# Kernel optimization log

Measured on AMD Instinct MI355X. Metric: run time of the kernel, lower is better.

The kernel has to match this reference:

```python
import jax, jax.numpy as jnp
import numpy as np
from jax.scipy.linalg import solve_triangular

JITTER = 1e-4  # matches init jitter


def kernel_ard(x1, x2, log_ls, log_sf):
    # ARD RBF kernel: sf * exp(-0.5 * || (x1 - x2) / ls ||^2)
    # x1: (b,H,N,D), x2: (b,H,M,D); log_ls: (H,D); log_sf: (H,1)
    inv_ls = jnp.exp(-log_ls)[None, :, None, :]
    a = x1 * inv_ls
    b = x2 * inv_ls
    d2 = (jnp.sum(a * a, -1)[..., :, None]
          - 2.0 * jnp.einsum('bhnd,bhmd->bhnm', a, b)
          + jnp.sum(b * b, -1)[..., None, :])
    sf = jnp.exp(log_sf)[None, :, :, None]  # (1,H,1,1)
    return sf * jnp.exp(-0.5 * d2)


def sgp_forward(x, cur_k, eps, W_qkv, log_sf, log_ls, v_ind, s_sqrt_ltri, log_s_sqrt_diag, W_O_w, W_O_b):
    B, L, hdim = x.shape
    H, vd = log_ls.shape
    M = cur_k.shape[1]
    S = eps.shape[2]

    # fc_qkv + head split (q and v_gamma interleaved per head)
    qkv = (x @ W_qkv.T).reshape(B, L, H, 2 * vd).transpose(0, 2, 1, 3)  # (B,H,L,2vd)
    q, v_gamma = qkv[..., :vd], qkv[..., vd:]

    # inducing keys: first hdim rows of fc_qkv weight applied to cur_k
    W_qk = W_qkv[:hdim].reshape(H, vd, hdim)
    k_beta = jnp.einsum('hdk,mk->hmd', W_qk, cur_k[0])[None]  # (1,H,M,vd)
    k_beta_b = jnp.broadcast_to(k_beta, (B, H, M, vd))
    v_beta = jnp.transpose(v_ind, (1, 0, 2, 3))               # (1,H,M,vd)
    log_ssqrt = jnp.transpose(log_s_sqrt_diag, (1, 0, 2, 3))  # (1,H,vd,M)

    K_qq = kernel_ard(q, q, log_ls, log_sf)               # (B,H,L,L)
    K_qk_beta = kernel_ard(q, k_beta_b, log_ls, log_sf)   # (B,H,L,M)
    K_kk = kernel_ard(k_beta, k_beta, log_ls, log_sf)     # (1,H,M,M)
    K_kq = jnp.swapaxes(K_qk_beta, -1, -2)                # (B,H,M,L)

    eyeM = jnp.eye(M, dtype=x.dtype)
    s_sqrt = jnp.exp(log_ssqrt)
    # diag_embed(s_sqrt) + strictly-lower-tri part of s_sqrt_ltri
    s_local = eyeM * s_sqrt[..., :, None] + jnp.tril(jnp.transpose(s_sqrt_ltri, (1, 0, 2, 3, 4)), -1)  # (1,H,vd,M,M)

    chol = jnp.linalg.cholesky(K_kk + JITTER * eyeM)      # (1,H,M,M)
    cholB = jnp.broadcast_to(chol, (B, H, M, M))
    v1 = solve_triangular(cholB, K_kq, lower=True)        # (B,H,M,L)
    v2 = solve_triangular(cholB, K_kq @ v_gamma, lower=True)  # (B,H,M,vd)
    v3 = jnp.einsum('bhml,hdmn->bhdln', v1, s_local[0])   # (B,H,vd,L,M)

    mean1 = K_qq @ v_gamma                                # (B,H,L,vd)
    mean = mean1 - jnp.einsum('bhml,bhmd->bhld', v1, v2) + K_qk_beta @ v_beta

    covar1 = jnp.diagonal(K_qq, axis1=-2, axis2=-1)[:, :, None, :, None]  # (B,H,1,L,1)
    v3sq = jnp.swapaxes(jnp.sum(v3 * v3, -1), 2, 3)[:, :, None]           # (B,H,1,L,vd)
    v1sq = jnp.sum(v1 * v1, 2)[:, :, None, :, None]                       # (B,H,1,L,1)
    chol_covar = jnp.sqrt(covar1 + v3sq - v1sq)           # (B,H,1,L,vd)

    samples = mean[:, :, None] + chol_covar * eps         # (B,H,S,L,vd)
    samples = samples.transpose(0, 2, 3, 1, 4).reshape(B, S, L, H * vd)
    out = samples @ W_O_w.T + W_O_b                       # (B,S,L,hdim); dropout p=0 -> identity

    # KL divergence (training path)
    kl = jnp.asarray(-0.5 * M * vd * H, dtype=x.dtype)
    kl = kl + 0.5 * jnp.sum(s_local * s_local)
    kl = kl + 0.5 * jnp.einsum('ohmd,ohmn,ohnd->', v_beta, K_kk, v_beta)
    per_b = jnp.sum(v_gamma * mean1, axis=(1, 2, 3)) - jnp.sum(v2 * v2, axis=(1, 2, 3))
    kl = kl + 0.5 * jnp.mean(per_b)
    kl = kl - jnp.sum(log_ssqrt)
    return out, kl


def setup_inputs():
    key = jax.random.key(0)
    ks = jax.random.split(key, 10)
    B, L, H, vd, M, S = 8, 512, 8, 64, 64, 2
    hdim = H * vd
    return {
        "x": jax.random.normal(ks[0], (B, L, hdim), jnp.float32),
        "cur_k": jax.random.normal(ks[1], (1, M, hdim), jnp.float32),
        "eps": jax.random.normal(ks[2], (B, H, S, L, vd), jnp.float32),
        "W_qkv": jax.random.normal(ks[3], (2 * hdim, hdim), jnp.float32) / np.float32(np.sqrt(hdim)),
        "log_sf": jnp.zeros((H, 1), jnp.float32),
        "log_ls": jax.random.normal(ks[4], (H, vd), jnp.float32),
        "v_ind": jax.random.normal(ks[5], (H, 1, M, vd), jnp.float32),
        "s_sqrt_ltri": 0.1 * jax.random.normal(ks[6], (H, 1, vd, M, M), jnp.float32),
        "log_s_sqrt_diag": jax.random.normal(ks[7], (H, 1, vd, M), jnp.float32),
        "W_O_w": jax.random.normal(ks[8], (hdim, hdim), jnp.float32) / np.float32(np.sqrt(hdim)),
        "W_O_b": jax.random.normal(ks[9], (hdim,), jnp.float32),
    }


def reference(x, cur_k, eps, W_qkv, log_sf, log_ls, v_ind, s_sqrt_ltri, log_s_sqrt_diag, W_O_w, W_O_b):
    return sgp_forward(x, cur_k, eps, W_qkv, log_sf, log_ls, v_ind, s_sqrt_ltri, log_s_sqrt_diag, W_O_w, W_O_b)
```

## Files before the change

kernel.cpp:

```cpp
#include <hip/hip_runtime.h>
#include <math.h>


using bf16x8 = __attribute__((ext_vector_type(8))) short;
using f32x4  = __attribute__((ext_vector_type(4))) float;

static const size_t OFF_QS   = 0;
static const size_t OFF_VG   = OFF_QS   + 2097152;
static const size_t OFF_QN   = OFF_VG   + 2097152;
static const size_t OFF_KBS  = OFF_QN   + 32768;
static const size_t OFF_KBN  = OFF_KBS  + 32768;
static const size_t OFF_LINV = OFF_KBN  + 512;
static const size_t OFF_V1   = OFF_LINV + 32768;
static const size_t OFF_V1SQ = OFF_V1   + 2097152;
static const size_t OFF_MEAN = OFF_V1SQ + 32768;
static const size_t OFF_V2   = OFF_MEAN + 2097152;
static const size_t OFF_V1H  = OFF_V2   + 262144;
static const size_t OFF_V1L  = OFF_V1H  + 1048576;
static const size_t OFF_STH  = OFF_V1L  + 1048576;
static const size_t OFF_STL  = OFF_STH  + 1048576;
static const size_t OFF_V3   = OFF_STL  + 1048576;
static const size_t OFF_WOH  = OFF_V3   + 2097152;
static const size_t OFF_WOL  = OFF_WOH  + 131072;
static const size_t OFF_KLD  = OFF_WOL  + 131072;

__device__ __forceinline__ unsigned short f2bf(float x) {
  unsigned u = __float_as_uint(x);
  u += 0x7FFFu + ((u >> 16) & 1u);
  return (unsigned short)(u >> 16);
}
__device__ __forceinline__ float bf2f(unsigned short s) {
  return __uint_as_float(((unsigned)s) << 16);
}
__device__ __forceinline__ void splitbf(float x, unsigned short& h, unsigned short& l) {
  h = f2bf(x);
  l = f2bf(x - bf2f(h));
}

__device__ __forceinline__ void load_tile_t(float* dst, const float* src, int ld) {
  int t = threadIdx.x;
  int r = t >> 2;
  int c0 = (t & 3) * 16;
#pragma unroll
  for (int q = 0; q < 4; ++q) {
    float4 v = *(const float4*)(src + (size_t)r * ld + c0 + q * 4);
    int c = c0 + q * 4;
    dst[(c + 0) * 68 + r] = v.x;
    dst[(c + 1) * 68 + r] = v.y;
    dst[(c + 2) * 68 + r] = v.z;
    dst[(c + 3) * 68 + r] = v.w;
  }
}
__device__ __forceinline__ void load_tile_n(float* dst, const float* src, int ld) {
  int t = threadIdx.x;
  int r = t >> 2;
  int c0 = (t & 3) * 16;
#pragma unroll
  for (int q = 0; q < 4; ++q) {
    float4 v = *(const float4*)(src + (size_t)r * ld + c0 + q * 4);
    *(float4*)(dst + r * 68 + c0 + q * 4) = v;
  }
}
__device__ __forceinline__ void mma64(const float* aT, const float* bT, int tr, int tn,
                                      float acc[4][4]) {
#pragma unroll 16
  for (int k = 0; k < 64; ++k) {
    float4 av = *(const float4*)(aT + k * 68 + tr);
    float4 bv = *(const float4*)(bT + k * 68 + tn);
    float a[4] = {av.x, av.y, av.z, av.w};
    float b[4] = {bv.x, bv.y, bv.z, bv.w};
#pragma unroll
    for (int i = 0; i < 4; ++i)
#pragma unroll
      for (int j = 0; j < 4; ++j) acc[i][j] = fmaf(a[i], b[j], acc[i][j]);
  }
}
__device__ __forceinline__ void mma64_dual(const float* aT, const float* b1T,
                                           const float* b2T, int tr, int tn,
                                           float acc1[4][4], float acc2[4][4]) {
#pragma unroll 8
  for (int k = 0; k < 64; ++k) {
    float4 av = *(const float4*)(aT + k * 68 + tr);
    float4 b1 = *(const float4*)(b1T + k * 68 + tn);
    float4 b2 = *(const float4*)(b2T + k * 68 + tn);
    float a[4] = {av.x, av.y, av.z, av.w};
    float p[4] = {b1.x, b1.y, b1.z, b1.w};
    float q[4] = {b2.x, b2.y, b2.z, b2.w};
#pragma unroll
    for (int i = 0; i < 4; ++i)
#pragma unroll
      for (int j = 0; j < 4; ++j) {
        acc1[i][j] = fmaf(a[i], p[j], acc1[i][j]);
        acc2[i][j] = fmaf(a[i], q[j], acc2[i][j]);
      }
  }
}

__global__ __launch_bounds__(256) void gemm0(
    const float* __restrict__ A, const float* __restrict__ Bm,
    float* __restrict__ qs, float* __restrict__ vg, const float* __restrict__ lls,
    float* __restrict__ qn) {
  __shared__ float As[16][68];
  __shared__ float Bs[16][68];
  const int t = threadIdx.x;
  const int r0 = blockIdx.x * 64;
  const int n0 = blockIdx.y * 64;
  const int lr = t >> 2;
  const int lk = (t & 3) * 4;
  const int tr = (t >> 4) * 4;
  const int tn = (t & 15) * 4;
  const float* Ap = A + (size_t)(r0 + lr) * 512 + lk;
  const float* Bp = Bm + (size_t)(n0 + lr) * 512 + lk;
  float acc[4][4] = {};
  for (int k0 = 0; k0 < 512; k0 += 16) {
    float4 a4 = *(const float4*)(Ap + k0);
    float4 b4 = *(const float4*)(Bp + k0);
    As[lk + 0][lr] = a4.x; As[lk + 1][lr] = a4.y; As[lk + 2][lr] = a4.z; As[lk + 3][lr] = a4.w;
    Bs[lk + 0][lr] = b4.x; Bs[lk + 1][lr] = b4.y; Bs[lk + 2][lr] = b4.z; Bs[lk + 3][lr] = b4.w;
    __syncthreads();
#pragma unroll
    for (int k = 0; k < 16; ++k) {
      float4 av = *(const float4*)&As[k][tr];
      float4 bv = *(const float4*)&Bs[k][tn];
      float a[4] = {av.x, av.y, av.z, av.w};
      float b[4] = {bv.x, bv.y, bv.z, bv.w};
#pragma unroll
      for (int i = 0; i < 4; ++i)
#pragma unroll
        for (int j = 0; j < 4; ++j) acc[i][j] = fmaf(a[i], b[j], acc[i][j]);
    }
    __syncthreads();
  }
  const int h = n0 >> 7;
  const bool isq = (n0 & 64) == 0;
  if (isq) {
    float invls[4];
#pragma unroll
    for (int j = 0; j < 4; ++j) invls[j] = __expf(-lls[h * 64 + tn + j]);
    float* red = &As[0][0];
#pragma unroll
    for (int i = 0; i < 4; ++i) {
      int r = r0 + tr + i;
      int b = r >> 9, l = r & 511;
      float4 o;
      o.x = acc[i][0] * invls[0];
      o.y = acc[i][1] * invls[1];
      o.z = acc[i][2] * invls[2];
      o.w = acc[i][3] * invls[3];
      *(float4*)(qs + (((size_t)(b * 8 + h)) * 512 + l) * 64 + tn) = o;
      red[(tr + i) * 17 + (t & 15)] = o.x * o.x + o.y * o.y + o.z * o.z + o.w * o.w;
    }
    __syncthreads();
    if (t < 64) {
      float s = 0.f;
#pragma unroll
      for (int g = 0; g < 16; ++g) s += red[t * 17 + g];
      int r = r0 + t;
      int b = r >> 9, l = r & 511;
      qn[(b * 8 + h) * 512 + l] = s;
    }
  } else {
#pragma unroll
    for (int i = 0; i < 4; ++i) {
      int r = r0 + tr + i;
      int b = r >> 9, l = r & 511;
      float4 o = {acc[i][0], acc[i][1], acc[i][2], acc[i][3]};
      *(float4*)(vg + (((size_t)(b * 8 + h)) * 512 + l) * 64 + tn) = o;
    }
  }
}

__global__ __launch_bounds__(256) void k2_kbeta(const float* __restrict__ W,
                                                const float* __restrict__ ckg,
                                                const float* __restrict__ log_ls,
                                                float* __restrict__ kbs,
                                                float* __restrict__ kbn) {
  __shared__ float ck[512];
  __shared__ float kb[64];
  int h = blockIdx.x >> 6, m = blockIdx.x & 63;
  int t = threadIdx.x;
  ck[t] = ckg[m * 512 + t];
  ck[t + 256] = ckg[m * 512 + t + 256];
  __syncthreads();
  int w = t >> 6, lane = t & 63;
  for (int d = w; d < 64; d += 4) {
    const float* row = W + (size_t)(h * 64 + d) * 512;
    float p = 0.f;
    for (int k = lane; k < 512; k += 64) p = fmaf(row[k], ck[k], p);
#pragma unroll
    for (int off = 32; off > 0; off >>= 1) p += __shfl_down(p, off);
    if (lane == 0) {
      float v = p * __expf(-log_ls[h * 64 + d]);
      kbs[(size_t)h * 4096 + m * 64 + d] = v;
      kb[d] = v;
    }
  }
  __syncthreads();
  if (w == 0) {
    float v = kb[lane];
    v *= v;
#pragma unroll
    for (int off = 32; off > 0; off >>= 1) v += __shfl_down(v, off);
    if (lane == 0) kbn[h * 64 + m] = v;
  }
}

__global__ __launch_bounds__(64) void k3_chol(const float* __restrict__ kbs,
                                              const float* __restrict__ kbn,
                                              const float* __restrict__ vind,
                                              const float* __restrict__ log_sf,
                                              float* __restrict__ linv_g,
                                              double* __restrict__ klbuf) {
  __shared__ float Am[64][65];
  __shared__ float Bm[64][65];
  __shared__ float kn[64];
  int h = blockIdx.x;
  int t = threadIdx.x;
  for (int m = 0; m < 64; ++m) Bm[m][t] = kbs[(size_t)h * 4096 + m * 64 + t];
  kn[t] = kbn[h * 64 + t];
  float lsf = log_sf[h];
  __syncthreads();
  float nh = -0.5f * kn[t] + lsf;
  for (int n = 0; n < 64; ++n) {
    float dt = 0.f;
#pragma unroll 8
    for (int d = 0; d < 64; ++d) dt = fmaf(Bm[t][d], Bm[n][d], dt);
    Am[t][n] = __expf(dt + nh - 0.5f * kn[n]);
  }
  __syncthreads();
  for (int m = 0; m < 64; ++m) Bm[m][t] = vind[(size_t)h * 4096 + m * 64 + t];
  __syncthreads();
  float s = 0.f;
  for (int m = 0; m < 64; ++m) {
    float tt = 0.f;
    for (int n = 0; n < 64; ++n) tt = fmaf(Am[m][n], Bm[n][t], tt);
    s = fmaf(Bm[m][t], tt, s);
  }
#pragma unroll
  for (int off = 32; off > 0; off >>= 1) s += __shfl_down(s, off);
  if (t == 0) atomicAdd(&klbuf[1], 0.5 * (double)s);
  __syncthreads();
  Am[t][t] += 1e-4f;
  __syncthreads();
  for (int k = 0; k < 64; ++k) {
    if (t == k) Am[k][k] = sqrtf(Am[k][k]);
    __syncthreads();
    if (t > k) Am[t][k] /= Am[k][k];
    __syncthreads();
    if (t > k) {
      float f = Am[t][k];
      for (int j = k + 1; j <= t; ++j) Am[t][j] = fmaf(-f, Am[j][k], Am[t][j]);
    }
    __syncthreads();
  }
  for (int i = 0; i < t; ++i) Bm[i][t] = 0.f;
  Bm[t][t] = 1.f / Am[t][t];
  for (int i = t + 1; i < 64; ++i) {
    float a = 0.f;
    for (int j = t; j < i; ++j) a = fmaf(Am[i][j], Bm[j][t], a);
    Bm[i][t] = -a / Am[i][i];
  }
  __syncthreads();
  for (int m = 0; m < 64; ++m) linv_g[(size_t)h * 4096 + m * 64 + t] = Bm[m][t];
}

__global__ __launch_bounds__(256) void ks_build(const float* __restrict__ ltri,
                                                const float* __restrict__ ldiag,
                                                unsigned short* __restrict__ sth,
                                                unsigned short* __restrict__ stl,
                                                double* __restrict__ klbuf) {
  __shared__ float r1[256], r2[256];
  int hd = blockIdx.x;
  int t = threadIdx.x;
  float p2 = 0.f, pl = 0.f;
  for (int i = t; i < 4096; i += 256) {
    int n = i >> 6, m = i & 63;
    float v;
    if (m == n) v = __expf(ldiag[hd * 64 + m]);
    else if (m > n) v = ltri[(size_t)hd * 4096 + m * 64 + n];
    else v = 0.f;
    unsigned short h, l;
    splitbf(v, h, l);
    sth[(size_t)hd * 4096 + i] = h;
    stl[(size_t)hd * 4096 + i] = l;
    p2 = fmaf(0.5f * v, v, p2);
  }
  if (t < 64) pl = ldiag[hd * 64 + t];
  r1[t] = p2;
  r2[t] = pl;
  __syncthreads();
  for (int sft = 128; sft > 0; sft >>= 1) {
    if (t < sft) { r1[t] += r1[t + sft]; r2[t] += r2[t + sft]; }
    __syncthreads();
  }
  if (t == 0) {
    atomicAdd(&klbuf[0], (double)r1[0]);
    atomicAdd(&klbuf[2], (double)r2[0]);
  }
}

__global__ __launch_bounds__(256) void kconv_wo(const float* __restrict__ w,
                                                unsigned short* __restrict__ wh,
                                                unsigned short* __restrict__ wl) {
  int i = blockIdx.x * 256 + threadIdx.x;
  float v = w[i];
  unsigned short h, l;
  splitbf(v, h, l);
  wh[i] = h;
  wl[i] = l;
}

__global__ __launch_bounds__(256) void k4_fused(
    const float* __restrict__ qs, const float* __restrict__ qn,
    const float* __restrict__ kbs, const float* __restrict__ kbn,
    const float* __restrict__ linv, const float* __restrict__ vind,
    const float* __restrict__ log_sf, float* __restrict__ v1,
    unsigned short* __restrict__ v1h, unsigned short* __restrict__ v1l,
    float* __restrict__ v1sq, float* __restrict__ meanbuf) {
  extern __shared__ float lds[];
  float* qsT = lds;
  float* kbT = lds + 4352;
  float* liT = lds + 2 * 4352;
  float* vbN = lds + 3 * 4352;
  float* red = lds + 4 * 4352;
  __shared__ float qn_s[64], kbn_s[64];
  const int lt = blockIdx.x, bh = blockIdx.y;
  const int h = bh & 7;
  const int t = threadIdx.x;
  const int l0 = lt * 64;
  const int tr = (t >> 4) * 4, tn = (t & 15) * 4;
  load_tile_t(qsT, qs + ((size_t)bh * 512 + l0) * 64, 64);
  load_tile_t(kbT, kbs + (size_t)h * 4096, 64);
  load_tile_t(liT, linv + (size_t)h * 4096, 64);
  load_tile_n(vbN, vind + (size_t)h * 4096, 64);
  if (t < 64) {
    qn_s[t] = qn[bh * 512 + l0 + t];
    kbn_s[t] = kbn[h * 64 + t];
  }
  __syncthreads();
  float acc[4][4] = {};
  mma64(qsT, kbT, tr, tn, acc);
  const float lsf = log_sf[h];
  float arow[4], acol[4];
#pragma unroll
  for (int i = 0; i < 4; ++i) arow[i] = -0.5f * qn_s[tr + i];
#pragma unroll
  for (int j = 0; j < 4; ++j) acol[j] = -0.5f * kbn_s[tn + j] + lsf;
  float kv[4][4];
#pragma unroll
  for (int i = 0; i < 4; ++i)
#pragma unroll
    for (int j = 0; j < 4; ++j) kv[i][j] = __expf(acc[i][j] + arow[i] + acol[j]);
  __syncthreads();
#pragma unroll
  for (int i = 0; i < 4; ++i)
#pragma unroll
    for (int j = 0; j < 4; ++j) qsT[(tn + j) * 68 + (tr + i)] = kv[i][j];
  __syncthreads();
  float a2[4][4] = {};
  float a3[4][4] = {};
  mma64_dual(qsT, liT, vbN, tr, tn, a2, a3);
#pragma unroll
  for (int i = 0; i < 4; ++i) {
    const size_t rowbase = ((size_t)bh * 512 + l0 + tr + i) * 64 + tn;
    float4 o = {a2[i][0], a2[i][1], a2[i][2], a2[i][3]};
    *(float4*)(v1 + rowbase) = o;
    short4 sh, sl;
    unsigned short hh, ll;
    splitbf(o.x, hh, ll); sh.x = (short)hh; sl.x = (short)ll;
    splitbf(o.y, hh, ll); sh.y = (short)hh; sl.y = (short)ll;
    splitbf(o.z, hh, ll); sh.z = (short)hh; sl.z = (short)ll;
    splitbf(o.w, hh, ll); sh.w = (short)hh; sl.w = (short)ll;
    *(short4*)(v1h + rowbase) = sh;
    *(short4*)(v1l + rowbase) = sl;
    red[(tr + i) * 17 + (t & 15)] =
        a2[i][0] * a2[i][0] + a2[i][1] * a2[i][1] + a2[i][2] * a2[i][2] + a2[i][3] * a2[i][3];
    float4 o3 = {a3[i][0], a3[i][1], a3[i][2], a3[i][3]};
    *(float4*)(meanbuf + rowbase) = o3;
  }
  __syncthreads();
  if (t < 64) {
    float s2 = 0.f;
#pragma unroll
    for (int g = 0; g < 16; ++g) s2 += red[t * 17 + g];
    v1sq[bh * 512 + l0 + t] = s2;
  }
}

__global__ __launch_bounds__(256) void k5_v2(const float* __restrict__ v1,
                                             const float* __restrict__ vg,
                                             float* __restrict__ v2,
                                             double* __restrict__ klbuf) {
  __shared__ float v1t[64 * 68];
  __shared__ float vgt[64 * 68];
  __shared__ float redp[256];
  const int bh = blockIdx.x;
  const int b = bh >> 3;
  const int t = threadIdx.x;
  const int tr = (t >> 4) * 4, tn = (t & 15) * 4;
  float acc[4][4] = {};
  for (int c0 = 0; c0 < 512; c0 += 64) {
    __syncthreads();
    load_tile_n(v1t, v1 + ((size_t)bh * 512 + c0) * 64, 64);
    load_tile_n(vgt, vg + ((size_t)bh * 512 + c0) * 64, 64);
    __syncthreads();
    mma64(v1t, vgt, tr, tn, acc);
  }
  float p = 0.f;
#pragma unroll
  for (int i = 0; i < 4; ++i) {
    float4 o = {acc[i][0], acc[i][1], acc[i][2], acc[i][3]};
    *(float4*)(v2 + ((size_t)bh * 64 + tr + i) * 64 + tn) = o;
    p += acc[i][0] * acc[i][0] + acc[i][1] * acc[i][1] + acc[i][2] * acc[i][2] +
         acc[i][3] * acc[i][3];
  }
  redp[t] = p;
  __syncthreads();
  if (t < 64) {
    float s = redp[t] + redp[t + 64] + redp[t + 128] + redp[t + 192];
#pragma unroll
    for (int off = 32; off > 0; off >>= 1) s += __shfl_down(s, off);
    if (t == 0) atomicAdd(&klbuf[11 + b], (double)s);
  }
}

__global__ __launch_bounds__(256) void k6_mean1(const float* __restrict__ qs,
                                                const float* __restrict__ qn,
                                                const float* __restrict__ vg,
                                                const float* __restrict__ log_sf,
                                                float* __restrict__ meanbuf,
                                                double* __restrict__ klbuf) {
  extern __shared__ float lds[];
  float* qrT = lds;
  float* qcT = lds + 4352;
  float* sT = lds + 2 * 4352;
  float* vgN = lds + 3 * 4352;
  __shared__ float qn_r[64], qn_c[64], redp[256];
  const int lt = blockIdx.x, bh = blockIdx.y;
  const int b = bh >> 3, h = bh & 7;
  const int l0 = lt * 64;
  const int t = threadIdx.x;
  const int tr = (t >> 4) * 4, tn = (t & 15) * 4;
  load_tile_t(qrT, qs + ((size_t)bh * 512 + l0) * 64, 64);
  if (t < 64) qn_r[t] = qn[bh * 512 + l0 + t];
  const float lsf = log_sf[h];
  float acc[4][4] = {};
  for (int c0 = 0; c0 < 512; c0 += 64) {
    __syncthreads();
    load_tile_t(qcT, qs + ((size_t)bh * 512 + c0) * 64, 64);
    load_tile_n(vgN, vg + ((size_t)bh * 512 + c0) * 64, 64);
    if (t < 64) qn_c[t] = qn[bh * 512 + c0 + t];
    __syncthreads();
    float dt[4][4] = {};
    mma64(qrT, qcT, tr, tn, dt);
    float arow[4], acol[4];
#pragma unroll
    for (int i = 0; i < 4; ++i) arow[i] = -0.5f * qn_r[tr + i];
#pragma unroll
    for (int j = 0; j < 4; ++j) acol[j] = -0.5f * qn_c[tn + j] + lsf;
#pragma unroll
    for (int i = 0; i < 4; ++i)
#pragma unroll
      for (int j = 0; j < 4; ++j)
        sT[(tn + j) * 68 + (tr + i)] = __expf(dt[i][j] + arow[i] + acol[j]);
    __syncthreads();
    mma64(sT, vgN, tr, tn, acc);
  }
  float pb = 0.f;
#pragma unroll
  for (int i = 0; i < 4; ++i) {
    size_t rowbase = ((size_t)bh * 512 + l0 + tr + i) * 64 + tn;
    float4 vgr = *(const float4*)(vg + rowbase);
    float4 mb = *(const float4*)(meanbuf + rowbase);
    pb += acc[i][0] * vgr.x + acc[i][1] * vgr.y + acc[i][2] * vgr.z + acc[i][3] * vgr.w;
    mb.x += acc[i][0]; mb.y += acc[i][1]; mb.z += acc[i][2]; mb.w += acc[i][3];
    *(float4*)(meanbuf + rowbase) = mb;
  }
  redp[t] = pb;
  __syncthreads();
  if (t < 64) {
    float s = redp[t] + redp[t + 64] + redp[t + 128] + redp[t + 192];
#pragma unroll
    for (int off = 32; off > 0; off >>= 1) s += __shfl_down(s, off);
    if (t == 0) atomicAdd(&klbuf[3 + b], (double)s);
  }
}

__global__ __launch_bounds__(256) void k10_mfma(const unsigned short* __restrict__ v1h,
                                                const unsigned short* __restrict__ sth,
                                                float* __restrict__ v3) {
  const int bh = blockIdx.x;
  const int l0 = blockIdx.y * 128;
  const int dz = blockIdx.z;
  const int h = bh & 7;
  const int t = threadIdx.x;
  const int wv = t >> 6;
  const int lane = t & 63;
  const int lr = lane & 15;
  const int kq = lane >> 4;
  const int lbase = l0 + wv * 32;
  bf16x8 a[2][2];
#pragma unroll
  for (int s = 0; s < 2; ++s)
#pragma unroll
    for (int kk = 0; kk < 2; ++kk)
      a[s][kk] = *(const bf16x8*)(v1h + ((size_t)bh * 512 + lbase + s * 16 + lr) * 64 +
                                  kk * 32 + kq * 8);
  const unsigned short* sbase = sth + (size_t)(h * 64 + dz * 16) * 4096;
  bf16x8 b[2][6];
#pragma unroll
  for (int ns = 0; ns < 4; ++ns)
    b[0][ns] = *(const bf16x8*)(sbase + (size_t)(ns * 16 + lr) * 64 + 32 + kq * 8);
#pragma unroll
  for (int ns = 0; ns < 2; ++ns)
    b[0][4 + ns] = *(const bf16x8*)(sbase + (size_t)(ns * 16 + lr) * 64 + kq * 8);
#pragma unroll
  for (int dd = 0; dd < 16; ++dd) {
    const int cur = dd & 1, nxt = cur ^ 1;
    if (dd < 15) {
      const unsigned short* sb = sbase + (size_t)(dd + 1) * 4096;
#pragma unroll
      for (int ns = 0; ns < 4; ++ns)
        b[nxt][ns] = *(const bf16x8*)(sb + (size_t)(ns * 16 + lr) * 64 + 32 + kq * 8);
#pragma unroll
      for (int ns = 0; ns < 2; ++ns)
        b[nxt][4 + ns] = *(const bf16x8*)(sb + (size_t)(ns * 16 + lr) * 64 + kq * 8);
    }
#pragma unroll
    for (int s = 0; s < 2; ++s) {
      f32x4 acc[4];
#pragma unroll
      for (int ns = 0; ns < 4; ++ns) acc[ns] = (f32x4){0.f, 0.f, 0.f, 0.f};
#pragma unroll
      for (int ns = 0; ns < 4; ++ns)
        acc[ns] = __builtin_amdgcn_mfma_f32_16x16x32_bf16(a[s][1], b[cur][ns], acc[ns], 0, 0, 0);
#pragma unroll
      for (int ns = 0; ns < 2; ++ns)
        acc[ns] = __builtin_amdgcn_mfma_f32_16x16x32_bf16(a[s][0], b[cur][4 + ns], acc[ns], 0, 0, 0);
      float sum[4];
#pragma unroll
      for (int r = 0; r < 4; ++r)
        sum[r] = acc[0][r] * acc[0][r] + acc[1][r] * acc[1][r] + acc[2][r] * acc[2][r] +
                 acc[3][r] * acc[3][r];
#pragma unroll
      for (int off = 1; off <= 8; off <<= 1)
#pragma unroll
        for (int r = 0; r < 4; ++r) sum[r] += __shfl_xor(sum[r], off);
      if (lr == 0) {
        const int d = dz * 16 + dd;
        const size_t base = ((size_t)(bh * 64 + d)) * 512 + lbase + s * 16 + kq * 4;
        v3[base + 0] = sum[0];
        v3[base + 1] = sum[1];
        v3[base + 2] = sum[2];
        v3[base + 3] = sum[3];
      }
    }
  }
}

__global__ __launch_bounds__(256) void k8_samples(
    const float* __restrict__ v1, const float* __restrict__ v2,
    const float* __restrict__ meanbuf, const float* __restrict__ v3,
    const float* __restrict__ v1sq, const float* __restrict__ eps,
    const float* __restrict__ log_sf, unsigned short* __restrict__ smph,
    unsigned short* __restrict__ smpl) {
  extern __shared__ float lds[];
  float* v1T = lds;
  float* v2N = lds + 4352;
  float* v3T = lds + 2 * 4352;
  __shared__ float v1sq_s[64];
  const int lt = blockIdx.x, bh = blockIdx.y;
  const int b = bh >> 3, h = bh & 7;
  const int l0 = lt * 64;
  const int t = threadIdx.x;
  const int tr = (t >> 4) * 4, tn = (t & 15) * 4;
  load_tile_t(v1T, v1 + ((size_t)bh * 512 + l0) * 64, 64);
  load_tile_n(v2N, v2 + (size_t)bh * 4096, 64);
  load_tile_n(v3T, v3 + (size_t)bh * 64 * 512 + l0, 512);
  if (t < 64) v1sq_s[t] = v1sq[bh * 512 + l0 + t];
  __syncthreads();
  float acc[4][4] = {};
  mma64(v1T, v2N, tr, tn, acc);
  const float sf = __expf(log_sf[h]);
#pragma unroll
  for (int i = 0; i < 4; ++i) {
    const int l = l0 + tr + i;
    size_t mbase = ((size_t)bh * 512 + l) * 64 + tn;
    float4 mb = *(const float4*)(meanbuf + mbase);
    float mean[4] = {mb.x - acc[i][0], mb.y - acc[i][1], mb.z - acc[i][2], mb.w - acc[i][3]};
    float cc[4];
#pragma unroll
    for (int j = 0; j < 4; ++j) {
      float var = sf + v3T[(tn + j) * 68 + (tr + i)] - v1sq_s[tr + i];
      cc[j] = sqrtf(fmaxf(var, 0.f));
    }
#pragma unroll
    for (int s2 = 0; s2 < 2; ++s2) {
      float4 ep = *(const float4*)(eps + (((size_t)bh * 2 + s2) * 512 + l) * 64 + tn);
      float o[4];
      o[0] = mean[0] + cc[0] * ep.x;
      o[1] = mean[1] + cc[1] * ep.y;
      o[2] = mean[2] + cc[2] * ep.z;
      o[3] = mean[3] + cc[3] * ep.w;
      short4 sh, sl;
      unsigned short hh, ll;
      splitbf(o[0], hh, ll); sh.x = (short)hh; sl.x = (short)ll;
      splitbf(o[1], hh, ll); sh.y = (short)hh; sl.y = (short)ll;
      splitbf(o[2], hh, ll); sh.z = (short)hh; sl.z = (short)ll;
      splitbf(o[3], hh, ll); sh.w = (short)hh; sl.w = (short)ll;
      const size_t obase = (((size_t)(b * 2 + s2) * 512 + l) * 512) + h * 64 + tn;
      *(short4*)(smph + obase) = sh;
      *(short4*)(smpl + obase) = sl;
    }
  }
}

__global__ __launch_bounds__(256) void gemm1_mfma(const unsigned short* __restrict__ smph,
                                                  const unsigned short* __restrict__ smpl,
                                                  const unsigned short* __restrict__ woh,
                                                  const unsigned short* __restrict__ wol,
                                                  const float* __restrict__ bias,
                                                  float* __restrict__ out) {
  const int r0 = blockIdx.x * 64;
  const int n0 = blockIdx.y * 64;
  const int t = threadIdx.x;
  const int wv = t >> 6;
  const int lane = t & 63;
  const int lr = lane & 15;
  const int kq = lane >> 4;
  const size_t arow = ((size_t)(r0 + wv * 16 + lr)) * 512;
  f32x4 acc[4];
#pragma unroll
  for (int ns = 0; ns < 4; ++ns) acc[ns] = (f32x4){0.f, 0.f, 0.f, 0.f};
  for (int ks = 0; ks < 16; ++ks) {
    const int kb = ks * 32 + kq * 8;
    bf16x8 ah = *(const bf16x8*)(smph + arow + kb);
    bf16x8 al = *(const bf16x8*)(smpl + arow + kb);
#pragma unroll
    for (int ns = 0; ns < 4; ++ns) {
      const size_t brow = ((size_t)(n0 + ns * 16 + lr)) * 512 + kb;
      bf16x8 bh8 = *(const bf16x8*)(woh + brow);
      bf16x8 bl8 = *(const bf16x8*)(wol + brow);
      acc[ns] = __builtin_amdgcn_mfma_f32_16x16x32_bf16(ah, bh8, acc[ns], 0, 0, 0);
      acc[ns] = __builtin_amdgcn_mfma_f32_16x16x32_bf16(ah, bl8, acc[ns], 0, 0, 0);
      acc[ns] = __builtin_amdgcn_mfma_f32_16x16x32_bf16(al, bh8, acc[ns], 0, 0, 0);
    }
  }
#pragma unroll
  for (int ns = 0; ns < 4; ++ns) {
    const int outc = n0 + ns * 16 + lr;
    const float bc = bias[outc];
    const int rbase = r0 + wv * 16 + kq * 4;
#pragma unroll
    for (int r = 0; r < 4; ++r) {
      out[(size_t)(rbase + r) * 512 + outc] = acc[ns][r] + bc;
    }
  }
}

__global__ void kfin(const double* __restrict__ klbuf, float* __restrict__ dout) {
  if (threadIdx.x == 0 && blockIdx.x == 0) {
    double pb = 0.0;
    for (int b = 0; b < 8; ++b) pb += klbuf[3 + b] - klbuf[11 + b];
    double kl = -16384.0 + klbuf[0] + klbuf[1] - klbuf[2] + pb / 16.0;
    dout[4194304] = (float)kl;
  }
}

extern "C" void kernel_launch(void* const* d_in, const int* in_sizes, int n_in,
                              void* d_out, int out_size, void* d_ws, size_t ws_size,
                              hipStream_t stream) {
  (void)in_sizes; (void)n_in; (void)out_size; (void)ws_size;
  const float* x     = (const float*)d_in[0];
  const float* cur_k = (const float*)d_in[1];
  const float* eps   = (const float*)d_in[2];
  const float* W_qkv = (const float*)d_in[3];
  const float* lsf   = (const float*)d_in[4];
  const float* lls   = (const float*)d_in[5];
  const float* vind  = (const float*)d_in[6];
  const float* ltri  = (const float*)d_in[7];
  const float* ldia  = (const float*)d_in[8];
  const float* Wo    = (const float*)d_in[9];
  const float* Wob   = (const float*)d_in[10];
  float* out = (float*)d_out;
  float* ws = (float*)d_ws;
  float* qs   = ws + OFF_QS;
  float* vg   = ws + OFF_VG;
  float* qn   = ws + OFF_QN;
  float* kbs  = ws + OFF_KBS;
  float* kbn  = ws + OFF_KBN;
  float* linv = ws + OFF_LINV;
  float* v1   = ws + OFF_V1;
  float* v1s  = ws + OFF_V1SQ;
  float* mean = ws + OFF_MEAN;
  float* v2   = ws + OFF_V2;
  float* v3   = ws + OFF_V3;
  unsigned short* v1h = (unsigned short*)(ws + OFF_V1H);
  unsigned short* v1l = (unsigned short*)(ws + OFF_V1L);
  unsigned short* sth = (unsigned short*)(ws + OFF_STH);
  unsigned short* stl = (unsigned short*)(ws + OFF_STL);
  unsigned short* woh = (unsigned short*)(ws + OFF_WOH);
  unsigned short* wol = (unsigned short*)(ws + OFF_WOL);
  unsigned short* smph = (unsigned short*)(ws + OFF_QS);
  unsigned short* smpl = (unsigned short*)(ws + OFF_VG);
  double* kld = (double*)(ws + OFF_KLD);

  hipMemsetAsync(kld, 0, 32 * sizeof(double), stream);
  gemm0<<<dim3(64, 16), 256, 0, stream>>>(x, W_qkv, qs, vg, lls, qn);
  k2_kbeta<<<512, 256, 0, stream>>>(W_qkv, cur_k, lls, kbs, kbn);
  k3_chol<<<8, 64, 0, stream>>>(kbs, kbn, vind, lsf, linv, kld);
  ks_build<<<512, 256, 0, stream>>>(ltri, ldia, sth, stl, kld);
  kconv_wo<<<1024, 256, 0, stream>>>(Wo, woh, wol);
  k4_fused<<<dim3(8, 64), 256, 73984, stream>>>(qs, qn, kbs, kbn, linv, vind, lsf,
                                                v1, v1h, v1l, v1s, mean);
  k5_v2<<<64, 256, 0, stream>>>(v1, vg, v2, kld);
  k6_mean1<<<dim3(8, 64), 256, 69632, stream>>>(qs, qn, vg, lsf, mean, kld);
  k10_mfma<<<dim3(64, 4, 4), 256, 0, stream>>>(v1h, sth, v3);
  k8_samples<<<dim3(8, 64), 256, 52224, stream>>>(v1, v2, mean, v3, v1s, eps, lsf,
                                                  smph, smpl);
  gemm1_mfma<<<dim3(128, 8), 256, 0, stream>>>(smph, smpl, woh, wol, Wob, out);
  kfin<<<1, 64, 0, stream>>>(kld, out);
}
```

Before: 611.9 us.

## Split Cholesky into parallel build and register-resident factor-invert; drop unused bf16 low parts

The single 64-thread Cholesky kernel becomes two kernels. A 256-thread kernel builds K_kk and the KL quadratic term with more parallelism. A second kernel does the Cholesky factorisation and computes the inverse at the same time, keeping each column in registers, so the serial triangular-inverse loop is gone. It also stops computing and storing the bf16 low-part buffers for v1 and S, which k10 apparently never read, cutting global writes. The extra launch and a round-trip through a kkk workspace buffer are the cost, along with heavy register use (128 floats per thread) in the factor kernel.

Measured after the change: 567.7 us. -7.2%, faster.

```diff
diff --git a/kernel.cpp b/kernel.cpp
--- a/kernel.cpp
+++ b/kernel.cpp
@@ -18,8 +18,9 @@
 static const size_t OFF_V1H  = OFF_V2   + 262144;
 static const size_t OFF_V1L  = OFF_V1H  + 1048576;
 static const size_t OFF_STH  = OFF_V1L  + 1048576;
-static const size_t OFF_STL  = OFF_STH  + 1048576;
-static const size_t OFF_V3   = OFF_STL  + 1048576;
+static const size_t OFF_KKK  = OFF_STH  + 1048576;
+static const size_t OFF_PAD0 = OFF_KKK  + 32768;
+static const size_t OFF_V3   = OFF_PAD0 + 1015808;
 static const size_t OFF_WOH  = OFF_V3   + 2097152;
 static const size_t OFF_WOL  = OFF_WOH  + 131072;
 static const size_t OFF_KLD  = OFF_WOL  + 131072;
@@ -205,69 +206,110 @@
   }
 }
 
-__global__ __launch_bounds__(64) void k3_chol(const float* __restrict__ kbs,
-                                              const float* __restrict__ kbn,
-                                              const float* __restrict__ vind,
-                                              const float* __restrict__ log_sf,
-                                              float* __restrict__ linv_g,
-                                              double* __restrict__ klbuf) {
-  __shared__ float Am[64][65];
-  __shared__ float Bm[64][65];
+__global__ __launch_bounds__(256) void k3a_build(const float* __restrict__ kbs,
+                                                 const float* __restrict__ kbn,
+                                                 const float* __restrict__ vind,
+                                                 const float* __restrict__ log_sf,
+                                                 float* __restrict__ kkk,
+                                                 double* __restrict__ klbuf) {
+  __shared__ float Bm[64 * 68];
+  __shared__ float Vb[64 * 68];
+  __shared__ float Am[64 * 68];
   __shared__ float kn[64];
-  int h = blockIdx.x;
-  int t = threadIdx.x;
-  for (int m = 0; m < 64; ++m) Bm[m][t] = kbs[(size_t)h * 4096 + m * 64 + t];
-  kn[t] = kbn[h * 64 + t];
-  float lsf = log_sf[h];
-  __syncthreads();
-  float nh = -0.5f * kn[t] + lsf;
-  for (int n = 0; n < 64; ++n) {
-    float dt = 0.f;
-#pragma unroll 8
-    for (int d = 0; d < 64; ++d) dt = fmaf(Bm[t][d], Bm[n][d], dt);
-    Am[t][n] = __expf(dt + nh - 0.5f * kn[n]);
-  }
-  __syncthreads();
-  for (int m = 0; m < 64; ++m) Bm[m][t] = vind[(size_t)h * 4096 + m * 64 + t];
-  __syncthreads();
-  float s = 0.f;
-  for (int m = 0; m < 64; ++m) {
-    float tt = 0.f;
-    for (int n = 0; n < 64; ++n) tt = fmaf(Am[m][n], Bm[n][t], tt);
-    s = fmaf(Bm[m][t], tt, s);
-  }
-#pragma unroll
-  for (int off = 32; off > 0; off >>= 1) s += __shfl_down(s, off);
-  if (t == 0) atomicAdd(&klbuf[1], 0.5 * (double)s);
-  __syncthreads();
-  Am[t][t] += 1e-4f;
-  __syncthreads();
+  __shared__ float redp[256];
+  const int h = blockIdx.x;
+  const int t = threadIdx.x;
+  load_tile_n(Bm, kbs + (size_t)h * 4096, 64);
+  load_tile_n(Vb, vind + (size_t)h * 4096, 64);
+  if (t < 64) kn[t] = kbn[h * 64 + t];
+  const float lsf = log_sf[h];
+  __syncthreads();
+  {
+    const int m = t >> 2, q = t & 3;
+    float rowm[64];
+#pragma unroll
+    for (int d = 0; d < 64; ++d) rowm[d] = Bm[m * 68 + d];
+    const float cm = -0.5f * kn[m] + lsf;
+#pragma unroll
+    for (int nn = 0; nn < 16; ++nn) {
+      const int n = q + nn * 4;
+      float dt = 0.f;
+#pragma unroll
+      for (int d = 0; d < 64; ++d) dt = fmaf(rowm[d], Bm[n * 68 + d], dt);
+      Am[m * 68 + n] = __expf(dt + cm - 0.5f * kn[n]);
+    }
+  }
+  __syncthreads();
+  {
+    const int d = t & 63, q2 = t >> 6;
+    float sp = 0.f;
+#pragma unroll
+    for (int mm = 0; mm < 16; ++mm) {
+      const int m = q2 * 16 + mm;
+      float tt = 0.f;
+#pragma unroll
+      for (int n = 0; n < 64; ++n) tt = fmaf(Am[m * 68 + n], Vb[n * 68 + d], tt);
+      sp = fmaf(Vb[m * 68 + d], tt, sp);
+    }
+    redp[t] = sp;
+  }
+  __syncthreads();
+  for (int sft = 128; sft > 0; sft >>= 1) {
+    if (t < sft) redp[t] += redp[t + sft];
+    __syncthreads();
+  }
+  if (t == 0) atomicAdd(&klbuf[1], 0.5 * (double)redp[0]);
+#pragma unroll
+  for (int rep = 0; rep < 16; ++rep) {
+    const int i = rep * 256 + t;
+    const int m = i >> 6, n = i & 63;
+    kkk[(size_t)h * 4096 + i] = Am[m * 68 + n] + (m == n ? 1e-4f : 0.f);
+  }
+}
+
+__global__ __launch_bounds__(64) void k3b_cholinv(const float* __restrict__ kkk,
+                                                  float* __restrict__ linv_g) {
+  __shared__ float colk[64];
+  __shared__ float rinv_s;
+  const int h = blockIdx.x;
+  const int t = threadIdx.x;
+  float a[64], x[64];
+#pragma unroll
+  for (int i = 0; i < 64; ++i) a[i] = kkk[(size_t)h * 4096 + i * 64 + t];
+#pragma unroll
+  for (int i = 0; i < 64; ++i) x[i] = (i == t) ? 1.f : 0.f;
+#pragma unroll
   for (int k = 0; k < 64; ++k) {
-    if (t == k) Am[k][k] = sqrtf(Am[k][k]);
-    __syncthreads();
-    if (t > k) Am[t][k] /= Am[k][k];
-    __syncthreads();
-    if (t > k) {
-      float f = Am[t][k];
-      for (int j = k + 1; j <= t; ++j) Am[t][j] = fmaf(-f, Am[j][k], Am[t][j]);
-    }
-    __syncthreads();
-  }
-  for (int i = 0; i < t; ++i) Bm[i][t] = 0.f;
-  Bm[t][t] = 1.f / Am[t][t];
-  for (int i = t + 1; i < 64; ++i) {
-    float a = 0.f;
-    for (int j = t; j < i; ++j) a = fmaf(Am[i][j], Bm[j][t], a);
-    Bm[i][t] = -a / Am[i][i];
-  }
-  __syncthreads();
-  for (int m = 0; m < 64; ++m) linv_g[(size_t)h * 4096 + m * 64 + t] = Bm[m][t];
+    if (t == k) {
+      const float dk = sqrtf(a[k]);
+      const float ri = 1.f / dk;
+      rinv_s = ri;
+#pragma unroll
+      for (int i = k + 1; i < 64; ++i) {
+        a[i] *= ri;
+        colk[i] = a[i];
+      }
+    }
+    __syncthreads();
+    const float ri = rinv_s;
+    const float fc = (t > k) ? colk[t] : 0.f;
+    const float xk = x[k] * ri;
+    x[k] = xk;
+#pragma unroll
+    for (int i = k + 1; i < 64; ++i) {
+      const float ci = colk[i];
+      a[i] = fmaf(-fc, ci, a[i]);
+      x[i] = fmaf(-ci, xk, x[i]);
+    }
+    __syncthreads();
+  }
+#pragma unroll
+  for (int m = 0; m < 64; ++m) linv_g[(size_t)h * 4096 + m * 64 + t] = x[m];
 }
 
 __global__ __launch_bounds__(256) void ks_build(const float* __restrict__ ltri,
                                                 const float* __restrict__ ldiag,
                                                 unsigned short* __restrict__ sth,
-                                                unsigned short* __restrict__ stl,
                                                 double* __restrict__ klbuf) {
   __shared__ float r1[256], r2[256];
   int hd = blockIdx.x;
@@ -279,10 +321,7 @@
     if (m == n) v = __expf(ldiag[hd * 64 + m]);
     else if (m > n) v = ltri[(size_t)hd * 4096 + m * 64 + n];
     else v = 0.f;
-    unsigned short h, l;
-    splitbf(v, h, l);
-    sth[(size_t)hd * 4096 + i] = h;
-    stl[(size_t)hd * 4096 + i] = l;
+    sth[(size_t)hd * 4096 + i] = f2bf(v);
     p2 = fmaf(0.5f * v, v, p2);
   }
   if (t < 64) pl = ldiag[hd * 64 + t];
@@ -315,7 +354,7 @@
     const float* __restrict__ kbs, const float* __restrict__ kbn,
     const float* __restrict__ linv, const float* __restrict__ vind,
     const float* __restrict__ log_sf, float* __restrict__ v1,
-    unsigned short* __restrict__ v1h, unsigned short* __restrict__ v1l,
+    unsigned short* __restrict__ v1h,
     float* __restrict__ v1sq, float* __restrict__ meanbuf) {
   extern __shared__ float lds[];
   float* qsT = lds;
@@ -365,14 +404,12 @@
     const size_t rowbase = ((size_t)bh * 512 + l0 + tr + i) * 64 + tn;
     float4 o = {a2[i][0], a2[i][1], a2[i][2], a2[i][3]};
     *(float4*)(v1 + rowbase) = o;
-    short4 sh, sl;
-    unsigned short hh, ll;
-    splitbf(o.x, hh, ll); sh.x = (short)hh; sl.x = (short)ll;
-    splitbf(o.y, hh, ll); sh.y = (short)hh; sl.y = (short)ll;
-    splitbf(o.z, hh, ll); sh.z = (short)hh; sl.z = (short)ll;
-    splitbf(o.w, hh, ll); sh.w = (short)hh; sl.w = (short)ll;
+    short4 sh;
+    sh.x = (short)f2bf(o.x);
+    sh.y = (short)f2bf(o.y);
+    sh.z = (short)f2bf(o.z);
+    sh.w = (short)f2bf(o.w);
     *(short4*)(v1h + rowbase) = sh;
-    *(short4*)(v1l + rowbase) = sl;
     red[(tr + i) * 17 + (t & 15)] =
         a2[i][0] * a2[i][0] + a2[i][1] * a2[i][1] + a2[i][2] * a2[i][2] + a2[i][3] * a2[i][3];
     float4 o3 = {a3[i][0], a3[i][1], a3[i][2], a3[i][3]};
@@ -694,11 +731,10 @@
   float* v1s  = ws + OFF_V1SQ;
   float* mean = ws + OFF_MEAN;
   float* v2   = ws + OFF_V2;
+  float* kkk  = ws + OFF_KKK;
   float* v3   = ws + OFF_V3;
   unsigned short* v1h = (unsigned short*)(ws + OFF_V1H);
-  unsigned short* v1l = (unsigned short*)(ws + OFF_V1L);
   unsigned short* sth = (unsigned short*)(ws + OFF_STH);
-  unsigned short* stl = (unsigned short*)(ws + OFF_STL);
   unsigned short* woh = (unsigned short*)(ws + OFF_WOH);
   unsigned short* wol = (unsigned short*)(ws + OFF_WOL);
   unsigned short* smph = (unsigned short*)(ws + OFF_QS);
@@ -708,11 +744,12 @@
   hipMemsetAsync(kld, 0, 32 * sizeof(double), stream);
   gemm0<<<dim3(64, 16), 256, 0, stream>>>(x, W_qkv, qs, vg, lls, qn);
   k2_kbeta<<<512, 256, 0, stream>>>(W_qkv, cur_k, lls, kbs, kbn);
-  k3_chol<<<8, 64, 0, stream>>>(kbs, kbn, vind, lsf, linv, kld);
-  ks_build<<<512, 256, 0, stream>>>(ltri, ldia, sth, stl, kld);
+  k3a_build<<<8, 256, 0, stream>>>(kbs, kbn, vind, lsf, kkk, kld);
+  k3b_cholinv<<<8, 64, 0, stream>>>(kkk, linv);
+  ks_build<<<512, 256, 0, stream>>>(ltri, ldia, sth, kld);
   kconv_wo<<<1024, 256, 0, stream>>>(Wo, woh, wol);
   k4_fused<<<dim3(8, 64), 256, 73984, stream>>>(qs, qn, kbs, kbn, linv, vind, lsf,
-                                                v1, v1h, v1l, v1s, mean);
+                                                v1, v1h, v1s, mean);
   k5_v2<<<64, 256, 0, stream>>>(v1, vg, v2, kld);
   k6_mean1<<<dim3(8, 64), 256, 69632, stream>>>(qs, qn, vg, lsf, mean, kld);
   k10_mfma<<<dim3(64, 4, 4), 256, 0, stream>>>(v1h, sth, v3);
```
